# Kernel optimization log

Measured on AMD Instinct MI355X. Metric: run time of the kernel, lower is better.

The kernel has to match this reference:

```python
import jax, jax.numpy as jnp
import numpy as np

K = 76          # model dim = 6 + 30 + 30 + 10 (concat of modality embeddings)
H = 8           # heads; per-head dim == K (wide attention variant)
D = 6           # depth
T = 1024        # seq_length (frames)
B = 8           # batch
C = 2           # num_classes
EPS = 1e-5


def setup_inputs() -> dict:
    key = jax.random.key(0)
    ks = jax.random.split(key, 24)
    rn = lambda k, shape, s=0.02: (jax.random.normal(k, shape, jnp.float32) * s)
    return {
        # forward inputs (per-frame multimodal features)
        "v": jax.random.normal(ks[0], (B, T, 6), jnp.float32),
        "x": jax.random.normal(ks[1], (B, T, 137), jnp.float32),
        "y": jax.random.normal(ks[2], (B, T, 113), jnp.float32),
        "z": jax.random.normal(ks[3], (B, T, 35), jnp.float32),
        # modality embed linears (stored (in, out); torch does x @ W.T)
        "W_hp": rn(ks[4], (6, 6)),     "b_hp": jnp.zeros((6,), jnp.float32),
        "W_lm": rn(ks[5], (137, 30)),  "b_lm": jnp.zeros((30,), jnp.float32),
        "W_el": rn(ks[6], (113, 30)),  "b_el": jnp.zeros((30,), jnp.float32),
        "W_au": rn(ks[7], (35, 10)),   "b_au": jnp.zeros((10,), jnp.float32),
        "pos_emb": rn(ks[8], (T, K)),
        # per-block params stacked over depth for lax.scan
        "Wq": rn(ks[9], (D, K, H * K)),
        "Wk": rn(ks[10], (D, K, H * K)),
        "Wv": rn(ks[11], (D, K, H * K)),
        "Wu": rn(ks[12], (D, H * K, K)), "bu": jnp.zeros((D, K), jnp.float32),
        "ln1_s": jnp.ones((D, K), jnp.float32), "ln1_b": jnp.zeros((D, K), jnp.float32),
        "W1": rn(ks[13], (D, K, 4 * K)), "b1": jnp.zeros((D, 4 * K), jnp.float32),
        "W2": rn(ks[14], (D, 4 * K, K)), "b2": jnp.zeros((D, K), jnp.float32),
        "ln2_s": jnp.ones((D, K), jnp.float32), "ln2_b": jnp.zeros((D, K), jnp.float32),
        "W_out": rn(ks[15], (K, C)), "b_out": jnp.zeros((C,), jnp.float32),
    }


def _layernorm(h, s, b):
    mu = jnp.mean(h, axis=-1, keepdims=True)
    var = jnp.mean(jnp.square(h - mu), axis=-1, keepdims=True)
    return (h - mu) * jax.lax.rsqrt(var + EPS) * s + b


def reference(v, x, y, z,
              W_hp, b_hp, W_lm, b_lm, W_el, b_el, W_au, b_au,
              pos_emb, Wq, Wk, Wv, Wu, bu, ln1_s, ln1_b,
              W1, b1, W2, b2, ln2_s, ln2_b, W_out, b_out):
    b, t = v.shape[0], v.shape[1]
    tokens = jnp.concatenate([
        v @ W_hp + b_hp,
        x @ W_lm + b_lm,
        y @ W_el + b_el,
        z @ W_au + b_au,
    ], axis=2)                                   # (b, t, K)
    h = tokens + pos_emb[None, :, :]
    scale = 1.0 / np.sqrt(K)                     # dot / sqrt(e), e == k

    def block(hh, p):
        wq, wk, wv, wu, bu_, l1s, l1b, w1, b1_, w2, b2_, l2s, l2b = p
        # (b, t, H*K) -> (b, H, t, K); per-head dim is full K here
        q = (hh @ wq).reshape(b, t, H, K).transpose(0, 2, 1, 3)
        k_ = (hh @ wk).reshape(b, t, H, K).transpose(0, 2, 1, 3)
        vv = (hh @ wv).reshape(b, t, H, K).transpose(0, 2, 1, 3)
        dot = jax.nn.softmax(jnp.einsum('bhte,bhse->bhts', q, k_) * scale, axis=-1)
        att = jnp.einsum('bhts,bhse->bhte', dot, vv)        # (b, H, t, K)
        att = att.transpose(0, 2, 1, 3).reshape(b, t, H * K)
        att = att @ wu + bu_                                # unify heads -> (b, t, K)
        h1 = _layernorm(att + hh, l1s, l1b)
        ff = jax.nn.relu(h1 @ w1 + b1_) @ w2 + b2_
        return _layernorm(ff + h1, l2s, l2b), None

    h, _ = jax.lax.scan(
        block, h,
        (Wq, Wk, Wv, Wu, bu, ln1_s, ln1_b, W1, b1, W2, b2, ln2_s, ln2_b))
    return h @ W_out + b_out                     # (b, t, num_classes)
```

## Files before the change

kernel.cpp:

```cpp
#include <hip/hip_runtime.h>
#include <hip/hip_bf16.h>
#include <math.h>

#define B_   8
#define T_   1024
#define K_   76
#define KP_  96
#define H_   8
#define D_   6
#define C_   2
#define HK_  608
#define QKLD_ 640
#define FF_  304
#define FFP_ 320
#define EK_  320
#define BT_  8192
#define EPS_ 1e-5f
#define SCL2_ (0.11470786693528088f * 1.4426950408889634f)

typedef unsigned short u16;
typedef unsigned int u32;
typedef short bf16x8 __attribute__((ext_vector_type(8)));
typedef float f32x4 __attribute__((ext_vector_type(4)));

__device__ __forceinline__ u16 f2b(float f) {
  __hip_bfloat16 h = __float2bfloat16(f);
  return *reinterpret_cast<u16*>(&h);
}
__device__ __forceinline__ float b2f(u16 u) {
  __hip_bfloat16 h = *reinterpret_cast<__hip_bfloat16*>(&u);
  return __bfloat162float(h);
}
__device__ __forceinline__ u32 pack2(float a, float b) {
  __hip_bfloat162 t = __float22bfloat162_rn(make_float2(a, b));
  return *reinterpret_cast<u32*>(&t);
}

#define PER_L_ 304128ULL
__global__ __launch_bounds__(256) void prep_kernel(
    const float* __restrict__ Wq, const float* __restrict__ Wk, const float* __restrict__ Wv,
    const float* __restrict__ Wu, const float* __restrict__ W1, const float* __restrict__ W2,
    u16* __restrict__ WT,
    const float* __restrict__ W_hp, const float* __restrict__ b_hp,
    const float* __restrict__ W_lm, const float* __restrict__ b_lm,
    const float* __restrict__ W_el, const float* __restrict__ b_el,
    const float* __restrict__ W_au, const float* __restrict__ b_au,
    u16* __restrict__ WE,
    const float* __restrict__ v, const float* __restrict__ x,
    const float* __restrict__ y, const float* __restrict__ z,
    u16* __restrict__ xin) {
  __shared__ float Ls[32][65];
  const int bid = blockIdx.x;
  if (bid < 1368) {
    int tile = bid % 38, zz = bid / 38;
    int d = zz / 6, wt = zz % 6;
    const float* in; int Kd, Nsrc, Nalloc, Kp; u16* out;
    size_t lb = (size_t)d * PER_L_;
    switch (wt) {
      case 0: in = Wq + (size_t)d*K_*HK_; Kd=K_;  Nsrc=HK_; Nalloc=640; Kp=KP_;  out = WT + lb;          break;
      case 1: in = Wk + (size_t)d*K_*HK_; Kd=K_;  Nsrc=HK_; Nalloc=640; Kp=KP_;  out = WT + lb + 61440;  break;
      case 2: in = Wv + (size_t)d*K_*HK_; Kd=K_;  Nsrc=HK_; Nalloc=640; Kp=KP_;  out = WT + lb + 122880; break;
      case 3: in = Wu + (size_t)d*HK_*K_; Kd=HK_; Nsrc=K_;  Nalloc=96;  Kp=HK_;  out = WT + lb + 184320; break;
      case 4: in = W1 + (size_t)d*K_*FF_; Kd=K_;  Nsrc=FF_; Nalloc=320; Kp=KP_;  out = WT + lb + 242688; break;
      default:in = W2 + (size_t)d*FF_*K_; Kd=FF_; Nsrc=K_;  Nalloc=96;  Kp=FFP_; out = WT + lb + 273408; break;
    }
    int tiles_k = Kp / 32;
    int tiles_n = (Nalloc + 63) / 64;
    if (tile >= tiles_k * tiles_n) return;
    int tn = tile / tiles_k, tk = tile % tiles_k;
    int n0 = tn * 64, k0 = tk * 32;
    for (int i = threadIdx.x; i < 2048; i += 256) {
      int kk = i >> 6, nn = i & 63;
      int gk = k0 + kk, gn = n0 + nn;
      int srccol = gn;
      if (wt < 3) {
        int hh8 = gn / 80, ft = gn - hh8 * 80;
        srccol = (ft < 76) ? (hh8 * 76 + ft) : -1;
      }
      Ls[kk][nn] = (gk < Kd && srccol >= 0 && srccol < Nsrc) ? in[(size_t)gk * Nsrc + srccol] : 0.f;
    }
    __syncthreads();
    for (int i = threadIdx.x; i < 2048; i += 256) {
      int nn = i >> 5, kk = i & 31;
      int gn = n0 + nn;
      if (gn < Nalloc) out[(size_t)gn * Kp + k0 + kk] = f2b(Ls[kk][nn]);
    }
  } else if (bid < 1488) {
    int idx = (bid - 1368) * 256 + threadIdx.x;
    if (idx >= 96 * EK_) return;
    int n = idx / EK_, kk = idx % EK_;
    float val = 0.f;
    if (n < 76) {
      if (kk < 6) { if (n < 6) val = W_hp[kk * 6 + n]; }
      else if (kk < 143) { int i = kk - 6; if (n >= 6 && n < 36) val = W_lm[i * 30 + (n - 6)]; }
      else if (kk < 256) { int i = kk - 143; if (n >= 36 && n < 66) val = W_el[i * 30 + (n - 36)]; }
      else if (kk < 291) { int i = kk - 256; if (n >= 66) val = W_au[i * 10 + (n - 66)]; }
      else if (kk == 291) {
        val = (n < 6) ? b_hp[n] : (n < 36) ? b_lm[n - 6] : (n < 66) ? b_el[n - 36] : b_au[n - 66];
      }
    }
    WE[idx] = f2b(val);
  } else {
    int idx = (bid - 1488) * 256 + threadIdx.x;
    if (idx >= BT_ * (EK_ / 2)) return;
    int bt = idx / (EK_ / 2), dc = idx % (EK_ / 2);
    int c0 = dc * 2;
    auto fetch = [&](int c) -> float {
      if (c < 6) return v[bt * 6 + c];
      if (c < 143) return x[bt * 137 + c - 6];
      if (c < 256) return y[bt * 113 + c - 143];
      if (c < 291) return z[bt * 35 + c - 256];
      if (c == 291) return 1.0f;
      return 0.f;
    };
    ((u32*)xin)[idx] = pack2(fetch(c0), fetch(c0 + 1));
  }
}

template<int RT, int CT, int KSTEPS, int RELU, int TPB>
__global__ __launch_bounds__(TPB) void gemm_kernel(
    const u16* __restrict__ A, int lda,
    const u16* __restrict__ Wt, int ldw, unsigned long long wstride,
    const float* __restrict__ bias,
    u16* __restrict__ Cc, int ldc, int N,
    int ksplit, int klen, unsigned long long osplit,
    float cs,
    u16* __restrict__ vbt,
    const float* __restrict__ pos) {
  __shared__ u16 Bs[CT * 16 * 56];
  const int tid = threadIdx.x;
  const int w = tid >> 6, lane = tid & 63;
  const int r = lane & 15, g = lane >> 4;
  const int n0 = blockIdx.x * CT * 16;
  const int m0 = blockIdx.y * (TPB / 64) * 16 * RT;
  const int z = blockIdx.z;
  const int k0 = z * ksplit;
  const int kend = k0 + klen;
  const u16* Wz = Wt + (size_t)z * wstride;
  const float* bias_eff = (z == 0) ? bias : nullptr;
  const float csz = (z == 0) ? cs : 1.f;
  u16* Cz = Cc + (size_t)z * osplit;
  constexpr int NB = (CT * 64 + TPB - 1) / TPB;

  const f32x4 fz = {0.f, 0.f, 0.f, 0.f};
  f32x4 acc[RT][CT];
  #pragma unroll
  for (int rt = 0; rt < RT; rt++)
    #pragma unroll
    for (int ct = 0; ct < CT; ct++) acc[rt][ct] = fz;

  bf16x8 a_all[RT][KSTEPS];
  #pragma unroll
  for (int rt = 0; rt < RT; rt++) {
    const u16* arow = A + (size_t)(m0 + (w * RT + rt) * 16 + r) * lda;
    #pragma unroll
    for (int ks = 0; ks < KSTEPS; ks++) {
      int kA = k0 + ks * 32 + g * 8;
      if (kA < kend) a_all[rt][ks] = *(const bf16x8*)(arow + kA);
      else a_all[rt][ks] = bf16x8{0, 0, 0, 0, 0, 0, 0, 0};
    }
  }

  uint4 bpre[NB];
  auto loadB = [&](int ks) {
    int kk = k0 + ks * 32;
    #pragma unroll
    for (int i0 = 0; i0 < NB; i0++) {
      int idx = tid + i0 * TPB;
      bpre[i0] = make_uint4(0, 0, 0, 0);
      if (idx < CT * 64) {
        int nn = idx >> 2, kc = idx & 3;
        if (kk + kc * 8 < kend)
          bpre[i0] = *(const uint4*)(Wz + (size_t)(n0 + nn) * ldw + kk + kc * 8);
      }
    }
  };
  loadB(0);

  for (int ks = 0; ks < KSTEPS; ks++) {
    __syncthreads();
    #pragma unroll
    for (int i0 = 0; i0 < NB; i0++) {
      int idx = tid + i0 * TPB;
      if (idx < CT * 64) {
        int nn = idx >> 2, kc = idx & 3;
        *(uint4*)&Bs[nn * 56 + (((kc ^ (nn & 3)) << 3))] = bpre[i0];
      }
    }
    __syncthreads();
    if (ks + 1 < KSTEPS) loadB(ks + 1);
    #pragma unroll
    for (int ct = 0; ct < CT; ct++) {
      bf16x8 bb = *(const bf16x8*)&Bs[(ct * 16 + r) * 56 + (((g ^ (r & 3)) << 3))];
      #pragma unroll
      for (int rt = 0; rt < RT; rt++)
        acc[rt][ct] = __builtin_amdgcn_mfma_f32_16x16x32_bf16(a_all[rt][ks], bb, acc[rt][ct], 0, 0, 0);
    }
  }

  if (vbt && z == 2) {
    #pragma unroll
    for (int rt = 0; rt < RT; rt++) {
      #pragma unroll
      for (int ct = 0; ct < CT; ct++) {
        int feat = ct * 16 + r;
        int token = m0 + (w * RT + rt) * 16 + g * 4;
        int bb_ = token >> 10, tt = token & 1023;
        ushort4 pk;
        if (feat < 76) {
          pk.x = f2b(acc[rt][ct][0]); pk.y = f2b(acc[rt][ct][1]);
          pk.z = f2b(acc[rt][ct][2]); pk.w = f2b(acc[rt][ct][3]);
        } else {
          pk = make_ushort4(0, 0, 0, 0);
        }
        *(ushort4*)(vbt + (((size_t)(bb_ * 8 + blockIdx.x) * 80 + feat) << 10) + tt) = pk;
      }
    }
  } else {
    #pragma unroll
    for (int rt = 0; rt < RT; rt++) {
      #pragma unroll
      for (int ct = 0; ct < CT; ct++) {
        int col = n0 + ct * 16 + r;
        if (col < ldc) {
          #pragma unroll
          for (int reg = 0; reg < 4; reg++) {
            int row = m0 + (w * RT + rt) * 16 + g * 4 + reg;
            float val = acc[rt][ct][reg] * csz;
            if (bias_eff && col < N) val += bias_eff[col];
            if (pos && col < N) val += pos[(row & (T_ - 1)) * K_ + col];
            if (RELU) val = fmaxf(val, 0.f);
            Cz[(size_t)row * ldc + col] = f2b(val);
          }
        }
      }
    }
  }
}

__global__ __launch_bounds__(64) void ffn_kernel(
    const u16* __restrict__ att, const u16* __restrict__ WuT, const float* __restrict__ bu,
    const u16* __restrict__ hres, const float* __restrict__ l1s, const float* __restrict__ l1b,
    const u16* __restrict__ W1T, const float* __restrict__ b1,
    const u16* __restrict__ W2T, const float* __restrict__ b2,
    const float* __restrict__ l2s, const float* __restrict__ l2b,
    u16* __restrict__ hout,
    const float* __restrict__ Wout, const float* __restrict__ bout,
    float* __restrict__ outp) {
  __shared__ u16 Bs[6 * 16 * 56];
  __shared__ u16 h1s[16 * 104];
  __shared__ u16 ffs[16 * 328];
  const int lane = threadIdx.x & 63;
  const int r = lane & 15, g = lane >> 4;
  const int m0 = blockIdx.x * 16;
  const f32x4 fz = {0.f, 0.f, 0.f, 0.f};

  u16 resv[4][6];
  #pragma unroll
  for (int reg = 0; reg < 4; reg++)
    #pragma unroll
    for (int ct = 0; ct < 6; ct++)
      resv[reg][ct] = hres[(size_t)(m0 + g * 4 + reg) * KP_ + ct * 16 + r];

  bf16x8 a1[19];
  {
    const u16* arow = att + (size_t)(m0 + r) * HK_;
    #pragma unroll
    for (int ks = 0; ks < 19; ks++) a1[ks] = *(const bf16x8*)(arow + ks * 32 + g * 8);
  }
  f32x4 acc1[6];
  #pragma unroll
  for (int ct = 0; ct < 6; ct++) acc1[ct] = fz;
  {
    uint4 bpre[6];
    auto loadB1 = [&](int ks) {
      #pragma unroll
      for (int i0 = 0; i0 < 6; i0++) {
        int idx = lane + i0 * 64;
        int nn = idx >> 2, kc = idx & 3;
        bpre[i0] = *(const uint4*)(WuT + (size_t)nn * HK_ + ks * 32 + kc * 8);
      }
    };
    loadB1(0);
    for (int ks = 0; ks < 19; ks++) {
      #pragma unroll
      for (int i0 = 0; i0 < 6; i0++) {
        int idx = lane + i0 * 64;
        int nn = idx >> 2, kc = idx & 3;
        *(uint4*)&Bs[nn * 56 + ((kc ^ (nn & 3)) << 3)] = bpre[i0];
      }
      if (ks + 1 < 19) loadB1(ks + 1);
      #pragma unroll
      for (int ct = 0; ct < 6; ct++) {
        bf16x8 bb = *(const bf16x8*)&Bs[(ct * 16 + r) * 56 + ((g ^ (r & 3)) << 3)];
        acc1[ct] = __builtin_amdgcn_mfma_f32_16x16x32_bf16(a1[ks], bb, acc1[ct], 0, 0, 0);
      }
    }
  }
  #pragma unroll
  for (int reg = 0; reg < 4; reg++) {
    float vals[6];
    float s = 0.f, s2 = 0.f;
    #pragma unroll
    for (int ct = 0; ct < 6; ct++) {
      int col = ct * 16 + r;
      float val = 0.f;
      if (col < K_) {
        val = acc1[ct][reg] + bu[col] + b2f(resv[reg][ct]);
        s += val; s2 += val * val;
      }
      vals[ct] = val;
    }
    #pragma unroll
    for (int m = 1; m < 16; m <<= 1) { s += __shfl_xor(s, m); s2 += __shfl_xor(s2, m); }
    float mu = s * (1.f / 76.f);
    float rstd = rsqrtf(s2 * (1.f / 76.f) - mu * mu + EPS_);
    #pragma unroll
    for (int ct = 0; ct < 6; ct++) {
      int col = ct * 16 + r;
      u16 ov = 0;
      if (col < K_) ov = f2b((vals[ct] - mu) * rstd * l1s[col] + l1b[col]);
      h1s[(g * 4 + reg) * 104 + col] = ov;
    }
  }

  bf16x8 a2[3];
  #pragma unroll
  for (int ks = 0; ks < 3; ks++)
    a2[ks] = *(const bf16x8*)&h1s[r * 104 + ks * 32 + g * 8];
  f32x4 acc2[20];
  #pragma unroll
  for (int ct = 0; ct < 20; ct++) acc2[ct] = fz;
  #pragma unroll
  for (int ks = 0; ks < 3; ks++) {
    bf16x8 bb[20];
    #pragma unroll
    for (int ct = 0; ct < 20; ct++)
      bb[ct] = *(const bf16x8*)(W1T + (size_t)(ct * 16 + r) * KP_ + ks * 32 + g * 8);
    #pragma unroll
    for (int ct = 0; ct < 20; ct++)
      acc2[ct] = __builtin_amdgcn_mfma_f32_16x16x32_bf16(a2[ks], bb[ct], acc2[ct], 0, 0, 0);
  }
  #pragma unroll
  for (int reg = 0; reg < 4; reg++)
    #pragma unroll
    for (int ct = 0; ct < 20; ct++) {
      int col = ct * 16 + r;
      float val = acc2[ct][reg] + ((col < FF_) ? b1[col] : 0.f);
      ffs[(g * 4 + reg) * 328 + col] = f2b(fmaxf(val, 0.f));
    }

  bf16x8 a3[10];
  #pragma unroll
  for (int ks = 0; ks < 10; ks++)
    a3[ks] = *(const bf16x8*)&ffs[r * 328 + ks * 32 + g * 8];
  f32x4 acc3[6];
  #pragma unroll
  for (int ct = 0; ct < 6; ct++) acc3[ct] = fz;
  {
    uint4 bpre[6];
    auto loadB3 = [&](int ks) {
      #pragma unroll
      for (int i0 = 0; i0 < 6; i0++) {
        int idx = lane + i0 * 64;
        int nn = idx >> 2, kc = idx & 3;
        bpre[i0] = *(const uint4*)(W2T + (size_t)nn * FFP_ + ks * 32 + kc * 8);
      }
    };
    loadB3(0);
    for (int ks = 0; ks < 10; ks++) {
      #pragma unroll
      for (int i0 = 0; i0 < 6; i0++) {
        int idx = lane + i0 * 64;
        int nn = idx >> 2, kc = idx & 3;
        *(uint4*)&Bs[nn * 56 + ((kc ^ (nn & 3)) << 3)] = bpre[i0];
      }
      if (ks + 1 < 10) loadB3(ks + 1);
      #pragma unroll
      for (int ct = 0; ct < 6; ct++) {
        bf16x8 bb = *(const bf16x8*)&Bs[(ct * 16 + r) * 56 + ((g ^ (r & 3)) << 3)];
        acc3[ct] = __builtin_amdgcn_mfma_f32_16x16x32_bf16(a3[ks], bb, acc3[ct], 0, 0, 0);
      }
    }
  }
  #pragma unroll
  for (int reg = 0; reg < 4; reg++) {
    float vals[6];
    float s = 0.f, s2 = 0.f;
    #pragma unroll
    for (int ct = 0; ct < 6; ct++) {
      int col = ct * 16 + r;
      float val = 0.f;
      if (col < K_) {
        val = acc3[ct][reg] + b2[col] + b2f(h1s[(g * 4 + reg) * 104 + col]);
        s += val; s2 += val * val;
      }
      vals[ct] = val;
    }
    #pragma unroll
    for (int m = 1; m < 16; m <<= 1) { s += __shfl_xor(s, m); s2 += __shfl_xor(s2, m); }
    float mu = s * (1.f / 76.f);
    float rstd = rsqrtf(s2 * (1.f / 76.f) - mu * mu + EPS_);
    u16* outr = hout + (size_t)(m0 + g * 4 + reg) * KP_;
    float p0 = 0.f, p1 = 0.f;
    #pragma unroll
    for (int ct = 0; ct < 6; ct++) {
      int col = ct * 16 + r;
      u16 ov = 0;
      if (col < K_) {
        float vln = (vals[ct] - mu) * rstd * l2s[col] + l2b[col];
        ov = f2b(vln);
        if (outp) {
          p0 += vln * Wout[col * 2];
          p1 += vln * Wout[col * 2 + 1];
        }
      }
      outr[col] = ov;
    }
    if (outp) {
      #pragma unroll
      for (int m = 1; m < 16; m <<= 1) { p0 += __shfl_xor(p0, m); p1 += __shfl_xor(p1, m); }
      if (r == 0) {
        int row = m0 + g * 4 + reg;
        outp[row * 2] = p0 + bout[0];
        outp[row * 2 + 1] = p1 + bout[1];
      }
    }
  }
}

__global__ __launch_bounds__(256, 3) void attn_kernel(const u16* __restrict__ q,
                                                      const u16* __restrict__ k,
                                                      const u16* __restrict__ vbt,
                                                      u16* __restrict__ att) {
  __shared__ u16 Ks[64 * 104];
  __shared__ u16 Vs[80 * 72];
  __shared__ u32 Psw[128 * 36];
  const int bid = blockIdx.x;
  const int hh = bid & 7, b = (bid >> 3) & 7, qt = bid >> 6;
  const int tid = threadIdx.x;
  const int w = tid >> 6, lane = tid & 63;
  const int r = lane & 15, g = lane >> 4;
  const int qbase = b * T_ + qt * 128;

  bf16x8 aq[2][3];
  #pragma unroll
  for (int rt = 0; rt < 2; rt++) {
    const u16* qsrc = q + (size_t)(qbase + w * 32 + rt * 16 + r) * QKLD_ + hh * 80;
    #pragma unroll
    for (int ks = 0; ks < 3; ks++) {
      int e0 = ks * 32 + g * 8;
      aq[rt][ks] = (e0 < 80) ? *(const bf16x8*)(qsrc + e0) : bf16x8{0, 0, 0, 0, 0, 0, 0, 0};
    }
  }

  const int krow = tid >> 2, kq4 = tid & 3;
  uint4 kpre[3], vpre[3];
  auto stage_load = [&](int kt) {
    const int kb = b * T_ + kt * 64;
    const u16* ksrc = k + (size_t)(kb + krow) * QKLD_ + hh * 80;
    #pragma unroll
    for (int i = 0; i < 3; i++) {
      int c = kq4 + 4 * i;
      kpre[i] = (c < 10) ? *(const uint4*)(ksrc + c * 8) : make_uint4(0, 0, 0, 0);
    }
    const u16* vsrc = vbt + (((size_t)(b * 8 + hh) * 80) << 10) + kt * 64;
    #pragma unroll
    for (int p = 0; p < 3; p++) {
      int idx = tid + p * 256;
      vpre[p] = (idx < 640) ? *(const uint4*)(vsrc + ((size_t)(idx >> 3) << 10) + (idx & 7) * 8)
                            : make_uint4(0, 0, 0, 0);
    }
  };
  auto stage_write = [&]() {
    #pragma unroll
    for (int i = 0; i < 3; i++) {
      int c = kq4 + 4 * i;
      *(uint4*)&Ks[krow * 104 + c * 8] = kpre[i];
    }
    #pragma unroll
    for (int p = 0; p < 3; p++) {
      int idx = tid + p * 256;
      if (idx < 640)
        *(uint4*)&Vs[(idx >> 3) * 72 + (idx & 7) * 8] = vpre[p];
    }
  };

  u32* Pw = Psw + w * 32 * 36;

  const f32x4 fz = {0.f, 0.f, 0.f, 0.f};
  f32x4 o[2][5];
  float ls[2] = {0.f, 0.f};
  #pragma unroll
  for (int rt = 0; rt < 2; rt++)
    #pragma unroll
    for (int i = 0; i < 5; i++) o[rt][i] = fz;

  stage_load(0);

  for (int kt = 0; kt < 16; kt++) {
    __syncthreads();
    stage_write();
    __syncthreads();
    if (kt < 15) stage_load(kt + 1);

    f32x4 st[2][4];
    #pragma unroll
    for (int ct = 0; ct < 4; ct++) { st[0][ct] = fz; st[1][ct] = fz; }
    __builtin_amdgcn_s_setprio(1);
    #pragma unroll
    for (int ct = 0; ct < 4; ct++) {
      #pragma unroll
      for (int ks = 0; ks < 3; ks++) {
        bf16x8 ak = *(const bf16x8*)&Ks[(ct * 16 + r) * 104 + ks * 32 + g * 8];
        st[0][ct] = __builtin_amdgcn_mfma_f32_16x16x32_bf16(ak, aq[0][ks], st[0][ct], 0, 0, 0);
        st[1][ct] = __builtin_amdgcn_mfma_f32_16x16x32_bf16(ak, aq[1][ks], st[1][ct], 0, 0, 0);
      }
    }
    __builtin_amdgcn_s_setprio(0);

    #pragma unroll
    for (int rt = 0; rt < 2; rt++) {
      float rs = 0.f;
      u32 pk[8];
      #pragma unroll
      for (int ct = 0; ct < 4; ct++) {
        float p0 = exp2f(st[rt][ct][0]), p1 = exp2f(st[rt][ct][1]);
        float p2 = exp2f(st[rt][ct][2]), p3 = exp2f(st[rt][ct][3]);
        rs += (p0 + p1) + (p2 + p3);
        pk[ct * 2] = pack2(p0, p1);
        pk[ct * 2 + 1] = pack2(p2, p3);
      }
      ls[rt] += rs;
      u32* pw = Pw + (rt * 16 + r) * 36;
      #pragma unroll
      for (int ct = 0; ct < 4; ct++)
        *(uint2*)(pw + ct * 8 + g * 2) = make_uint2(pk[ct * 2], pk[ct * 2 + 1]);
    }

    bf16x8 pa[2][2];
    #pragma unroll
    for (int rt = 0; rt < 2; rt++) {
      const u32* pr = Pw + (rt * 16 + r) * 36;
      #pragma unroll
      for (int ks = 0; ks < 2; ks++) {
        uint4 t = *(const uint4*)(pr + ks * 16 + g * 4);
        pa[rt][ks] = *reinterpret_cast<bf16x8*>(&t);
      }
    }
    __builtin_amdgcn_s_setprio(1);
    #pragma unroll
    for (int ks = 0; ks < 2; ks++) {
      #pragma unroll
      for (int c5 = 0; c5 < 5; c5++) {
        bf16x8 av = *(const bf16x8*)&Vs[(c5 * 16 + r) * 72 + ks * 32 + g * 8];
        #pragma unroll
        for (int rt = 0; rt < 2; rt++)
          o[rt][c5] = __builtin_amdgcn_mfma_f32_16x16x32_bf16(av, pa[rt][ks], o[rt][c5], 0, 0, 0);
      }
    }
    __builtin_amdgcn_s_setprio(0);
  }

  #pragma unroll
  for (int rt = 0; rt < 2; rt++) {
    ls[rt] += __shfl_xor(ls[rt], 16);
    ls[rt] += __shfl_xor(ls[rt], 32);
    float inv = 1.f / ls[rt];
    int token = qbase + w * 32 + rt * 16 + r;
    #pragma unroll
    for (int c5 = 0; c5 < 5; c5++) {
      if (c5 == 4 && g == 3) continue;
      ushort4 pk4;
      pk4.x = f2b(o[rt][c5][0] * inv);
      pk4.y = f2b(o[rt][c5][1] * inv);
      pk4.z = f2b(o[rt][c5][2] * inv);
      pk4.w = f2b(o[rt][c5][3] * inv);
      *(ushort4*)&att[(size_t)token * HK_ + hh * 76 + c5 * 16 + g * 4] = pk4;
    }
  }
}

extern "C" void kernel_launch(void* const* d_in, const int* in_sizes, int n_in,
                              void* d_out, int out_size, void* d_ws, size_t ws_size,
                              hipStream_t stream) {
  const float* v    = (const float*)d_in[0];
  const float* x    = (const float*)d_in[1];
  const float* y    = (const float*)d_in[2];
  const float* z    = (const float*)d_in[3];
  const float* W_hp = (const float*)d_in[4];
  const float* b_hp = (const float*)d_in[5];
  const float* W_lm = (const float*)d_in[6];
  const float* b_lm = (const float*)d_in[7];
  const float* W_el = (const float*)d_in[8];
  const float* b_el = (const float*)d_in[9];
  const float* W_au = (const float*)d_in[10];
  const float* b_au = (const float*)d_in[11];
  const float* pos  = (const float*)d_in[12];
  const float* Wq   = (const float*)d_in[13];
  const float* Wk   = (const float*)d_in[14];
  const float* Wv   = (const float*)d_in[15];
  const float* Wu   = (const float*)d_in[16];
  const float* bu   = (const float*)d_in[17];
  const float* ln1s = (const float*)d_in[18];
  const float* ln1b = (const float*)d_in[19];
  const float* W1   = (const float*)d_in[20];
  const float* b1   = (const float*)d_in[21];
  const float* W2   = (const float*)d_in[22];
  const float* b2   = (const float*)d_in[23];
  const float* ln2s = (const float*)d_in[24];
  const float* ln2b = (const float*)d_in[25];
  const float* Wout = (const float*)d_in[26];
  const float* bout = (const float*)d_in[27];

  u16* ws  = (u16*)d_ws;
  u16* WT  = ws;
  u16* WE  = WT + 1824768;
  u16* h   = WE + 30720;
  u16* xin = h + 786432;
  u16* qb  = xin + 2621440;
  u16* kb  = qb + 5242880;
  u16* vbt = kb + 5242880;
  u16* att = vbt + 5242880;

  prep_kernel<<<dim3(6608), 256, 0, stream>>>(
      Wq, Wk, Wv, Wu, W1, W2, WT,
      W_hp, b_hp, W_lm, b_lm, W_el, b_el, W_au, b_au, WE,
      v, x, y, z, xin);
  gemm_kernel<1, 6, 10, 0, 128><<<dim3(1, 256, 1), 128, 0, stream>>>(
      xin, EK_, WE, EK_, 0ULL, nullptr, h, KP_, K_, 0, EK_, 0ULL,
      1.f, nullptr, pos);

  for (int d = 0; d < D_; d++) {
    u16* WTd = WT + (size_t)d * PER_L_;
    const float* bu_d = bu + (size_t)d * K_;
    const float* l1s  = ln1s + (size_t)d * K_;
    const float* l1b  = ln1b + (size_t)d * K_;
    const float* b1_d = b1 + (size_t)d * FF_;
    const float* b2_d = b2 + (size_t)d * K_;
    const float* l2s  = ln2s + (size_t)d * K_;
    const float* l2b  = ln2b + (size_t)d * K_;

    gemm_kernel<2, 5, 3, 0, 256><<<dim3(8, 64, 3), 256, 0, stream>>>(
        h, KP_, WTd, KP_, 61440ULL, nullptr, qb, QKLD_, QKLD_, 0, KP_, 5242880ULL,
        SCL2_, vbt, nullptr);
    attn_kernel<<<dim3(512), 256, 0, stream>>>(qb, kb, vbt, att);
    ffn_kernel<<<dim3(512), 64, 0, stream>>>(
        att, WTd + 184320, bu_d, h, l1s, l1b,
        WTd + 242688, b1_d, WTd + 273408, b2_d, l2s, l2b, h,
        Wout, bout, (d == D_ - 1) ? (float*)d_out : nullptr);
  }
}
```

Measured before the change: 514.1 us.

## Split FFN kernel across two waves with split-K reduction through shared memory

The fused unify/FFN kernel now runs two wavefronts per 16-row block instead of one. The Wu and W2 GEMMs are split along K between the waves, with the partial accumulators summed through shared memory, and the W1 GEMM is split by output columns. The aim is more parallelism and latency hiding for a kernel that launches only 512 single-wave blocks. In exchange it adds syncthreads, a shared-memory reduction and a second Bs buffer. Wave 1 zeroes the A operand of its first K step, which overlaps wave 0's last step, so that step is not counted twice.

```diff
diff --git a/kernel.cpp b/kernel.cpp
--- a/kernel.cpp
+++ b/kernel.cpp
@@ -238,7 +238,7 @@
   }
 }
 
-__global__ __launch_bounds__(64) void ffn_kernel(
+__global__ __launch_bounds__(128) void ffn_kernel(
     const u16* __restrict__ att, const u16* __restrict__ WuT, const float* __restrict__ bu,
     const u16* __restrict__ hres, const float* __restrict__ l1s, const float* __restrict__ l1b,
     const u16* __restrict__ W1T, const float* __restrict__ b1,
@@ -247,183 +247,219 @@
     u16* __restrict__ hout,
     const float* __restrict__ Wout, const float* __restrict__ bout,
     float* __restrict__ outp) {
-  __shared__ u16 Bs[6 * 16 * 56];
+  __shared__ u16 Bs[2][5376];
   __shared__ u16 h1s[16 * 104];
   __shared__ u16 ffs[16 * 328];
-  const int lane = threadIdx.x & 63;
+  const int tid = threadIdx.x;
+  const int wv = tid >> 6, lane = tid & 63;
   const int r = lane & 15, g = lane >> 4;
   const int m0 = blockIdx.x * 16;
   const f32x4 fz = {0.f, 0.f, 0.f, 0.f};
+  u16* Bw = Bs[wv];
+  float* scr = (float*)Bs[1];
 
   u16 resv[4][6];
-  #pragma unroll
-  for (int reg = 0; reg < 4; reg++)
-    #pragma unroll
-    for (int ct = 0; ct < 6; ct++)
-      resv[reg][ct] = hres[(size_t)(m0 + g * 4 + reg) * KP_ + ct * 16 + r];
-
-  bf16x8 a1[19];
+  if (wv == 0) {
+    #pragma unroll
+    for (int reg = 0; reg < 4; reg++)
+      #pragma unroll
+      for (int ct = 0; ct < 6; ct++)
+        resv[reg][ct] = hres[(size_t)(m0 + g * 4 + reg) * KP_ + ct * 16 + r];
+  }
+
+  const int ks0 = wv * 9;
+  bf16x8 a1[10];
   {
     const u16* arow = att + (size_t)(m0 + r) * HK_;
     #pragma unroll
-    for (int ks = 0; ks < 19; ks++) a1[ks] = *(const bf16x8*)(arow + ks * 32 + g * 8);
+    for (int i = 0; i < 10; i++) {
+      if (wv && i == 0) a1[i] = bf16x8{0, 0, 0, 0, 0, 0, 0, 0};
+      else a1[i] = *(const bf16x8*)(arow + (ks0 + i) * 32 + g * 8);
+    }
   }
   f32x4 acc1[6];
   #pragma unroll
   for (int ct = 0; ct < 6; ct++) acc1[ct] = fz;
   {
     uint4 bpre[6];
-    auto loadB1 = [&](int ks) {
+    auto loadB1 = [&](int ksAbs) {
       #pragma unroll
       for (int i0 = 0; i0 < 6; i0++) {
         int idx = lane + i0 * 64;
         int nn = idx >> 2, kc = idx & 3;
-        bpre[i0] = *(const uint4*)(WuT + (size_t)nn * HK_ + ks * 32 + kc * 8);
+        bpre[i0] = *(const uint4*)(WuT + (size_t)nn * HK_ + ksAbs * 32 + kc * 8);
       }
     };
-    loadB1(0);
-    for (int ks = 0; ks < 19; ks++) {
+    loadB1(ks0);
+    #pragma unroll
+    for (int i = 0; i < 10; i++) {
       #pragma unroll
       for (int i0 = 0; i0 < 6; i0++) {
         int idx = lane + i0 * 64;
         int nn = idx >> 2, kc = idx & 3;
-        *(uint4*)&Bs[nn * 56 + ((kc ^ (nn & 3)) << 3)] = bpre[i0];
-      }
-      if (ks + 1 < 19) loadB1(ks + 1);
+        *(uint4*)&Bw[nn * 56 + ((kc ^ (nn & 3)) << 3)] = bpre[i0];
+      }
+      if (i + 1 < 10) loadB1(ks0 + i + 1);
       #pragma unroll
       for (int ct = 0; ct < 6; ct++) {
-        bf16x8 bb = *(const bf16x8*)&Bs[(ct * 16 + r) * 56 + ((g ^ (r & 3)) << 3)];
-        acc1[ct] = __builtin_amdgcn_mfma_f32_16x16x32_bf16(a1[ks], bb, acc1[ct], 0, 0, 0);
-      }
-    }
-  }
-  #pragma unroll
-  for (int reg = 0; reg < 4; reg++) {
-    float vals[6];
-    float s = 0.f, s2 = 0.f;
-    #pragma unroll
-    for (int ct = 0; ct < 6; ct++) {
-      int col = ct * 16 + r;
-      float val = 0.f;
-      if (col < K_) {
-        val = acc1[ct][reg] + bu[col] + b2f(resv[reg][ct]);
-        s += val; s2 += val * val;
-      }
-      vals[ct] = val;
-    }
-    #pragma unroll
-    for (int m = 1; m < 16; m <<= 1) { s += __shfl_xor(s, m); s2 += __shfl_xor(s2, m); }
-    float mu = s * (1.f / 76.f);
-    float rstd = rsqrtf(s2 * (1.f / 76.f) - mu * mu + EPS_);
-    #pragma unroll
-    for (int ct = 0; ct < 6; ct++) {
-      int col = ct * 16 + r;
-      u16 ov = 0;
-      if (col < K_) ov = f2b((vals[ct] - mu) * rstd * l1s[col] + l1b[col]);
-      h1s[(g * 4 + reg) * 104 + col] = ov;
-    }
-  }
-
-  bf16x8 a2[3];
-  #pragma unroll
-  for (int ks = 0; ks < 3; ks++)
-    a2[ks] = *(const bf16x8*)&h1s[r * 104 + ks * 32 + g * 8];
-  f32x4 acc2[20];
-  #pragma unroll
-  for (int ct = 0; ct < 20; ct++) acc2[ct] = fz;
-  #pragma unroll
-  for (int ks = 0; ks < 3; ks++) {
-    bf16x8 bb[20];
-    #pragma unroll
-    for (int ct = 0; ct < 20; ct++)
-      bb[ct] = *(const bf16x8*)(W1T + (size_t)(ct * 16 + r) * KP_ + ks * 32 + g * 8);
-    #pragma unroll
-    for (int ct = 0; ct < 20; ct++)
-      acc2[ct] = __builtin_amdgcn_mfma_f32_16x16x32_bf16(a2[ks], bb[ct], acc2[ct], 0, 0, 0);
-  }
-  #pragma unroll
-  for (int reg = 0; reg < 4; reg++)
-    #pragma unroll
-    for (int ct = 0; ct < 20; ct++) {
-      int col = ct * 16 + r;
-      float val = acc2[ct][reg] + ((col < FF_) ? b1[col] : 0.f);
-      ffs[(g * 4 + reg) * 328 + col] = f2b(fmaxf(val, 0.f));
-    }
-
-  bf16x8 a3[10];
-  #pragma unroll
-  for (int ks = 0; ks < 10; ks++)
-    a3[ks] = *(const bf16x8*)&ffs[r * 328 + ks * 32 + g * 8];
+        bf16x8 bb = *(const bf16x8*)&Bw[(ct * 16 + r) * 56 + ((g ^ (r & 3)) << 3)];
+        acc1[ct] = __builtin_amdgcn_mfma_f32_16x16x32_bf16(a1[i], bb, acc1[ct], 0, 0, 0);
+      }
+    }
+  }
+  if (wv == 1) {
+    #pragma unroll
+    for (int ct = 0; ct < 6; ct++)
+      *(f32x4*)(scr + lane * 24 + ct * 4) = acc1[ct];
+  }
+  __syncthreads();
+  if (wv == 0) {
+    #pragma unroll
+    for (int ct = 0; ct < 6; ct++) acc1[ct] += *(const f32x4*)(scr + lane * 24 + ct * 4);
+    #pragma unroll
+    for (int reg = 0; reg < 4; reg++) {
+      float vals[6];
+      float s = 0.f, s2 = 0.f;
+      #pragma unroll
+      for (int ct = 0; ct < 6; ct++) {
+        int col = ct * 16 + r;
+        float val = 0.f;
+        if (col < K_) {
+          val = acc1[ct][reg] + bu[col] + b2f(resv[reg][ct]);
+          s += val; s2 += val * val;
+        }
+        vals[ct] = val;
+      }
+      #pragma unroll
+      for (int m = 1; m < 16; m <<= 1) { s += __shfl_xor(s, m); s2 += __shfl_xor(s2, m); }
+      float mu = s * (1.f / 76.f);
+      float rstd = rsqrtf(s2 * (1.f / 76.f) - mu * mu + EPS_);
+      #pragma unroll
+      for (int ct = 0; ct < 6; ct++) {
+        int col = ct * 16 + r;
+        u16 ov = 0;
+        if (col < K_) ov = f2b((vals[ct] - mu) * rstd * l1s[col] + l1b[col]);
+        h1s[(g * 4 + reg) * 104 + col] = ov;
+      }
+    }
+  }
+  __syncthreads();
+
+  {
+    bf16x8 a2[3];
+    #pragma unroll
+    for (int ks = 0; ks < 3; ks++)
+      a2[ks] = *(const bf16x8*)&h1s[r * 104 + ks * 32 + g * 8];
+    f32x4 acc2[10];
+    #pragma unroll
+    for (int ct = 0; ct < 10; ct++) acc2[ct] = fz;
+    #pragma unroll
+    for (int ks = 0; ks < 3; ks++) {
+      bf16x8 bb[10];
+      #pragma unroll
+      for (int ct = 0; ct < 10; ct++)
+        bb[ct] = *(const bf16x8*)(W1T + (size_t)((wv * 10 + ct) * 16 + r) * KP_ + ks * 32 + g * 8);
+      #pragma unroll
+      for (int ct = 0; ct < 10; ct++)
+        acc2[ct] = __builtin_amdgcn_mfma_f32_16x16x32_bf16(a2[ks], bb[ct], acc2[ct], 0, 0, 0);
+    }
+    #pragma unroll
+    for (int reg = 0; reg < 4; reg++)
+      #pragma unroll
+      for (int ct = 0; ct < 10; ct++) {
+        int col = (wv * 10 + ct) * 16 + r;
+        float val = acc2[ct][reg] + ((col < FF_) ? b1[col] : 0.f);
+        ffs[(g * 4 + reg) * 328 + col] = f2b(fmaxf(val, 0.f));
+      }
+  }
+  __syncthreads();
+
+  const int k3 = wv * 5;
+  bf16x8 a3[5];
+  #pragma unroll
+  for (int i = 0; i < 5; i++)
+    a3[i] = *(const bf16x8*)&ffs[r * 328 + (k3 + i) * 32 + g * 8];
   f32x4 acc3[6];
   #pragma unroll
   for (int ct = 0; ct < 6; ct++) acc3[ct] = fz;
   {
     uint4 bpre[6];
-    auto loadB3 = [&](int ks) {
+    auto loadB3 = [&](int ksAbs) {
       #pragma unroll
       for (int i0 = 0; i0 < 6; i0++) {
         int idx = lane + i0 * 64;
         int nn = idx >> 2, kc = idx & 3;
-        bpre[i0] = *(const uint4*)(W2T + (size_t)nn * FFP_ + ks * 32 + kc * 8);
+        bpre[i0] = *(const uint4*)(W2T + (size_t)nn * FFP_ + ksAbs * 32 + kc * 8);
       }
     };
-    loadB3(0);
-    for (int ks = 0; ks < 10; ks++) {
+    loadB3(k3);
+    #pragma unroll
+    for (int i = 0; i < 5; i++) {
       #pragma unroll
       for (int i0 = 0; i0 < 6; i0++) {
         int idx = lane + i0 * 64;
         int nn = idx >> 2, kc = idx & 3;
-        *(uint4*)&Bs[nn * 56 + ((kc ^ (nn & 3)) << 3)] = bpre[i0];
-      }
-      if (ks + 1 < 10) loadB3(ks + 1);
+        *(uint4*)&Bw[nn * 56 + ((kc ^ (nn & 3)) << 3)] = bpre[i0];
+      }
+      if (i + 1 < 5) loadB3(k3 + i + 1);
       #pragma unroll
       for (int ct = 0; ct < 6; ct++) {
-        bf16x8 bb = *(const bf16x8*)&Bs[(ct * 16 + r) * 56 + ((g ^ (r & 3)) << 3)];
-        acc3[ct] = __builtin_amdgcn_mfma_f32_16x16x32_bf16(a3[ks], bb, acc3[ct], 0, 0, 0);
-      }
-    }
-  }
-  #pragma unroll
-  for (int reg = 0; reg < 4; reg++) {
-    float vals[6];
-    float s = 0.f, s2 = 0.f;
-    #pragma unroll
-    for (int ct = 0; ct < 6; ct++) {
-      int col = ct * 16 + r;
-      float val = 0.f;
-      if (col < K_) {
-        val = acc3[ct][reg] + b2[col] + b2f(h1s[(g * 4 + reg) * 104 + col]);
-        s += val; s2 += val * val;
-      }
-      vals[ct] = val;
-    }
-    #pragma unroll
-    for (int m = 1; m < 16; m <<= 1) { s += __shfl_xor(s, m); s2 += __shfl_xor(s2, m); }
-    float mu = s * (1.f / 76.f);
-    float rstd = rsqrtf(s2 * (1.f / 76.f) - mu * mu + EPS_);
-    u16* outr = hout + (size_t)(m0 + g * 4 + reg) * KP_;
-    float p0 = 0.f, p1 = 0.f;
-    #pragma unroll
-    for (int ct = 0; ct < 6; ct++) {
-      int col = ct * 16 + r;
-      u16 ov = 0;
-      if (col < K_) {
-        float vln = (vals[ct] - mu) * rstd * l2s[col] + l2b[col];
-        ov = f2b(vln);
-        if (outp) {
-          p0 += vln * Wout[col * 2];
-          p1 += vln * Wout[col * 2 + 1];
+        bf16x8 bb = *(const bf16x8*)&Bw[(ct * 16 + r) * 56 + ((g ^ (r & 3)) << 3)];
+        acc3[ct] = __builtin_amdgcn_mfma_f32_16x16x32_bf16(a3[i], bb, acc3[ct], 0, 0, 0);
+      }
+    }
+  }
+  if (wv == 1) {
+    #pragma unroll
+    for (int ct = 0; ct < 6; ct++)
+      *(f32x4*)(scr + lane * 24 + ct * 4) = acc3[ct];
+  }
+  __syncthreads();
+  if (wv == 0) {
+    #pragma unroll
+    for (int ct = 0; ct < 6; ct++) acc3[ct] += *(const f32x4*)(scr + lane * 24 + ct * 4);
+    #pragma unroll
+    for (int reg = 0; reg < 4; reg++) {
+      float vals[6];
+      float s = 0.f, s2 = 0.f;
+      #pragma unroll
+      for (int ct = 0; ct < 6; ct++) {
+        int col = ct * 16 + r;
+        float val = 0.f;
+        if (col < K_) {
+          val = acc3[ct][reg] + b2[col] + b2f(h1s[(g * 4 + reg) * 104 + col]);
+          s += val; s2 += val * val;
         }
-      }
-      outr[col] = ov;
-    }
-    if (outp) {
-      #pragma unroll
-      for (int m = 1; m < 16; m <<= 1) { p0 += __shfl_xor(p0, m); p1 += __shfl_xor(p1, m); }
-      if (r == 0) {
-        int row = m0 + g * 4 + reg;
-        outp[row * 2] = p0 + bout[0];
-        outp[row * 2 + 1] = p1 + bout[1];
+        vals[ct] = val;
+      }
+      #pragma unroll
+      for (int m = 1; m < 16; m <<= 1) { s += __shfl_xor(s, m); s2 += __shfl_xor(s2, m); }
+      float mu = s * (1.f / 76.f);
+      float rstd = rsqrtf(s2 * (1.f / 76.f) - mu * mu + EPS_);
+      u16* outr = hout + (size_t)(m0 + g * 4 + reg) * KP_;
+      float p0 = 0.f, p1 = 0.f;
+      #pragma unroll
+      for (int ct = 0; ct < 6; ct++) {
+        int col = ct * 16 + r;
+        u16 ov = 0;
+        if (col < K_) {
+          float vln = (vals[ct] - mu) * rstd * l2s[col] + l2b[col];
+          ov = f2b(vln);
+          if (outp) {
+            p0 += vln * Wout[col * 2];
+            p1 += vln * Wout[col * 2 + 1];
+          }
+        }
+        outr[col] = ov;
+      }
+      if (outp) {
+        #pragma unroll
+        for (int m = 1; m < 16; m <<= 1) { p0 += __shfl_xor(p0, m); p1 += __shfl_xor(p1, m); }
+        if (r == 0) {
+          int row = m0 + g * 4 + reg;
+          outp[row * 2] = p0 + bout[0];
+          outp[row * 2 + 1] = p1 + bout[1];
+        }
       }
     }
   }
@@ -645,7 +681,7 @@
         h, KP_, WTd, KP_, 61440ULL, nullptr, qb, QKLD_, QKLD_, 0, KP_, 5242880ULL,
         SCL2_, vbt, nullptr);
     attn_kernel<<<dim3(512), 256, 0, stream>>>(qb, kb, vbt, att);
-    ffn_kernel<<<dim3(512), 64, 0, stream>>>(
+    ffn_kernel<<<dim3(512), 128, 0, stream>>>(
         att, WTd + 184320, bu_d, h, l1s, l1b,
         WTd + 242688, b1_d, WTd + 273408, b2_d, l2s, l2b, h,
         Wout, bout, (d == D_ - 1) ? (float*)d_out : nullptr);
```

Result: slower. 551.3 us (+7.3%).
